# Kernel optimization log

Hardware: AMD Instinct MI355X
Metric: run time of the kernel (lower is better)

Reference implementation:

```python
import jax, jax.numpy as jnp
import numpy as np

D_IN = 1024
D_OUT = 1024
NUM_HEADS = 16
HEAD_DIM = D_OUT // NUM_HEADS


def setup_inputs() -> dict:
    key = jax.random.key(0)
    k_x, k_q, k_k, k_v, k_o, k_ob = jax.random.split(key, 6)
    s_in = 1.0 / np.sqrt(D_IN)
    s_out = 1.0 / np.sqrt(D_OUT)
    return {
        "x": jax.random.normal(k_x, (2, 2048, D_IN), dtype=jnp.float32),
        "W_q": jax.random.uniform(k_q, (D_IN, D_OUT), minval=-s_in, maxval=s_in, dtype=jnp.float32),
        "W_k": jax.random.uniform(k_k, (D_IN, D_OUT), minval=-s_in, maxval=s_in, dtype=jnp.float32),
        "W_v": jax.random.uniform(k_v, (D_IN, D_OUT), minval=-s_in, maxval=s_in, dtype=jnp.float32),
        "W_out": jax.random.uniform(k_o, (D_OUT, D_OUT), minval=-s_out, maxval=s_out, dtype=jnp.float32),
        "b_out": jax.random.uniform(k_ob, (D_OUT,), minval=-s_out, maxval=s_out, dtype=jnp.float32),
    }


def reference(x, W_q, W_k, W_v, W_out, b_out):
    b, t, _ = x.shape
    # projections (qkv_bias=False)
    q = (x @ W_q).reshape(b, t, NUM_HEADS, HEAD_DIM).transpose(0, 2, 1, 3)  # [b,h,t,d]
    k = (x @ W_k).reshape(b, t, NUM_HEADS, HEAD_DIM).transpose(0, 2, 1, 3)
    v = (x @ W_v).reshape(b, t, NUM_HEADS, HEAD_DIM).transpose(0, 2, 1, 3)
    scale = 1.0 / np.sqrt(HEAD_DIM).astype(np.float32)
    scores = jnp.einsum("bhqd,bhkd->bhqk", q, k) * scale  # [b,h,t,t]
    causal = jnp.triu(jnp.ones((t, t), dtype=bool), k=1)
    scores = jnp.where(causal, -jnp.inf, scores)
    weights = jax.nn.softmax(scores, axis=-1)
    # dropout p=0.0 -> identity
    context = jnp.einsum("bhqk,bhkd->bhqd", weights, v)
    context = context.transpose(0, 2, 1, 3).reshape(b, t, D_OUT)
    return context @ W_out + b_out
```

## Files before the change

kernel.cpp:

```cpp
#include <hip/hip_runtime.h>
#include <hip/hip_bf16.h>

#define B_  2
#define T_  2048
#define D_  1024
#define H_  16
#define DH_ 64
#define M_  (B_*T_)

typedef _Float16 f16;
typedef __attribute__((ext_vector_type(4))) _Float16 f16x4;
typedef __attribute__((ext_vector_type(8))) _Float16 f16x8;
typedef __attribute__((ext_vector_type(4))) float f32x4;

#define GLOAD_LDS(gp, lp) __builtin_amdgcn_global_load_lds( \
    (const __attribute__((address_space(1))) void*)(gp),    \
    (__attribute__((address_space(3))) void*)(lp), 16, 0, 0)

__global__ void cvt_x(const float* __restrict__ x, f16* __restrict__ xb) {
  size_t i = ((size_t)blockIdx.x * blockDim.x + threadIdx.x) * 8;
  float4 a = *(const float4*)(x + i);
  float4 b = *(const float4*)(x + i + 4);
  f16x8 o;
  o[0]=(f16)a.x; o[1]=(f16)a.y; o[2]=(f16)a.z; o[3]=(f16)a.w;
  o[4]=(f16)b.x; o[5]=(f16)b.y; o[6]=(f16)b.z; o[7]=(f16)b.w;
  *(f16x8*)(xb + i) = o;
}

__global__ void twt(const float* __restrict__ wq, const float* __restrict__ wk,
                    const float* __restrict__ wv, const float* __restrict__ wo,
                    f16* __restrict__ wqkvT, f16* __restrict__ woutT) {
  int j = blockIdx.z;
  const float* src = (j==0)?wq:(j==1)?wk:(j==2)?wv:wo;
  f16* dst = (j<3) ? (wqkvT + (size_t)j*D_*D_) : woutT;
  __shared__ float tile[32][33];
  int n0 = blockIdx.x*32, k0 = blockIdx.y*32;
  int tx = threadIdx.x, ty = threadIdx.y;
  #pragma unroll
  for (int i=0;i<32;i+=8)
    tile[ty+i][tx] = src[(size_t)(k0+ty+i)*D_ + n0+tx];
  __syncthreads();
  #pragma unroll
  for (int i=0;i<32;i+=8)
    dst[(size_t)(n0+ty+i)*D_ + k0+tx] = (f16)tile[tx][ty+i];
}

__launch_bounds__(256, 2)
__global__ void qkv_gemm(const f16* __restrict__ xb, const f16* __restrict__ wT,
                         f16* __restrict__ Qp, f16* __restrict__ Kp, f16* __restrict__ Vtp) {
  const int j  = blockIdx.z;
  const f16* B0 = wT + (size_t)j * D_ * D_;
  const int m0 = blockIdx.y * 128;
  const int n0 = blockIdx.x * 128;
  __shared__ alignas(16) char smem[128*136*2];
  f16* AsF = (f16*)smem;
  f16* BsF = AsF + 128*64;
  const int tid = threadIdx.x;
  const int lane = tid & 63, wave = tid >> 6;
  const int ln = lane & 15, quad = lane >> 4;
  const int wm = wave >> 1, wn = wave & 1;

  f32x4 acc[4][4];
  #pragma unroll
  for (int a=0;a<4;++a)
    #pragma unroll
    for (int b=0;b<4;++b) acc[a][b] = f32x4{0.f,0.f,0.f,0.f};

  for (int k0 = 0; k0 < D_; k0 += 64) {
    #pragma unroll
    for (int p = 0; p < 4; ++p) {
      int slot = p*256 + tid;
      int row  = slot >> 3;
      int c    = (slot & 7) ^ (row & 7);
      GLOAD_LDS(xb + (size_t)(m0+row)*D_ + k0 + c*8, AsF + (size_t)slot*8);
      GLOAD_LDS(B0 + (size_t)(n0+row)*D_ + k0 + c*8, BsF + (size_t)slot*8);
    }
    __syncthreads();
    #pragma unroll
    for (int ks = 0; ks < 2; ++ks) {
      const int cb = ((ks*4 + quad) ^ (ln & 7)) * 8;
      f16x8 af[4], bf[4];
      #pragma unroll
      for (int mt = 0; mt < 4; ++mt)
        af[mt] = *(const f16x8*)(AsF + (size_t)(wm*64 + mt*16 + ln)*64 + cb);
      #pragma unroll
      for (int nt = 0; nt < 4; ++nt)
        bf[nt] = *(const f16x8*)(BsF + (size_t)(wn*64 + nt*16 + ln)*64 + cb);
      #pragma unroll
      for (int mt = 0; mt < 4; ++mt)
        #pragma unroll
        for (int nt = 0; nt < 4; ++nt)
          acc[mt][nt] = __builtin_amdgcn_mfma_f32_16x16x32_f16(af[mt], bf[nt], acc[mt][nt], 0, 0, 0);
    }
    __syncthreads();
  }

  if (j < 2) {
    #pragma unroll
    for (int mt = 0; mt < 4; ++mt)
      #pragma unroll
      for (int nt = 0; nt < 4; ++nt)
        #pragma unroll
        for (int r = 0; r < 4; ++r) {
          int gm = m0 + wm*64 + mt*16 + quad*4 + r;
          int gn = n0 + wn*64 + nt*16 + ln;
          int bb = gm >> 11, t = gm & (T_-1);
          int h  = gn >> 6,  dd = gn & (DH_-1);
          float v = acc[mt][nt][r];
          size_t idx = ((((size_t)bb*H_ + h)*T_ + t)*DH_) + dd;
          if (j == 0) Qp[idx] = (f16)(v * 0.125f);
          else        Kp[idx] = (f16)v;
        }
  } else {
    __syncthreads();
    f16* VtS = (f16*)smem;
    #pragma unroll
    for (int mt = 0; mt < 4; ++mt)
      #pragma unroll
      for (int nt = 0; nt < 4; ++nt) {
        f16x4 v;
        v[0]=(f16)acc[mt][nt][0]; v[1]=(f16)acc[mt][nt][1];
        v[2]=(f16)acc[mt][nt][2]; v[3]=(f16)acc[mt][nt][3];
        *(f16x4*)&VtS[(size_t)(wn*64 + nt*16 + ln)*136 + wm*64 + mt*16 + quad*4] = v;
      }
    __syncthreads();
    int dd_loc = tid >> 1, half = tid & 1;
    int gn = n0 + dd_loc, h = gn >> 6, dd = gn & (DH_-1);
    int bb = m0 >> 11, tb = (m0 & (T_-1)) + half*64;
    f16* dst = Vtp + ((size_t)(bb*H_ + h)*DH_ + dd)*T_ + tb;
    const f16* src = VtS + (size_t)dd_loc*136 + half*64;
    #pragma unroll
    for (int u = 0; u < 8; ++u)
      *(uint4*)(dst + u*8) = *(const uint4*)(src + u*8);
  }
}

__launch_bounds__(256, 4)
__global__ void flash(const f16* __restrict__ Qp, const f16* __restrict__ Kp,
                      const f16* __restrict__ Vtp, f16* __restrict__ ctx) {
  const int xi = blockIdx.x;
  const int qt = (xi & 1) ? ((xi - 1) >> 1) : (31 - (xi >> 1));
  const int bh = blockIdx.y;
  const int b = bh >> 4, h = bh & (H_-1);
  const size_t headQK = (size_t)bh * T_ * DH_;
  const size_t headV  = (size_t)bh * DH_ * T_;
  const int tid = threadIdx.x, lane = tid & 63, w = tid >> 6;
  const int ln = lane & 15, quad = lane >> 4;
  __shared__ alignas(16) f16 Ks[64][72];
  __shared__ alignas(16) f16 Vs[64][72];
  __shared__ alignas(16) f16 Ps[64][72];

  const int qw = qt*64 + w*16;

  f16x8 qf[2];
  #pragma unroll
  for (int ks = 0; ks < 2; ++ks)
    qf[ks] = *(const f16x8*)&Qp[headQK + (size_t)(qw + ln)*DH_ + ks*32 + quad*8];

  f32x4 o[4];
  #pragma unroll
  for (int dt = 0; dt < 4; ++dt) o[dt] = f32x4{0.f,0.f,0.f,0.f};
  float l_part = 0.f;

  const int srow = tid >> 2, scol = (tid & 3) * 16;
  for (int it = 0; it <= qt; ++it) {
    const int kv0 = it * 64;
    *(uint4*)&Ks[srow][scol]   = *(const uint4*)&Kp[headQK + (size_t)(kv0+srow)*DH_ + scol];
    *(uint4*)&Ks[srow][scol+8] = *(const uint4*)&Kp[headQK + (size_t)(kv0+srow)*DH_ + scol + 8];
    *(uint4*)&Vs[srow][scol]   = *(const uint4*)&Vtp[headV + (size_t)srow*T_ + kv0 + scol];
    *(uint4*)&Vs[srow][scol+8] = *(const uint4*)&Vtp[headV + (size_t)srow*T_ + kv0 + scol + 8];
    __syncthreads();

    f32x4 s[4];
    #pragma unroll
    for (int kt = 0; kt < 4; ++kt) s[kt] = f32x4{0.f,0.f,0.f,0.f};
    #pragma unroll
    for (int ks = 0; ks < 2; ++ks) {
      f16x8 kx[4];
      #pragma unroll
      for (int kt = 0; kt < 4; ++kt)
        kx[kt] = *(const f16x8*)&Ks[kt*16 + ln][ks*32 + quad*8];
      #pragma unroll
      for (int kt = 0; kt < 4; ++kt)
        s[kt] = __builtin_amdgcn_mfma_f32_16x16x32_f16(kx[kt], qf[ks], s[kt], 0, 0, 0);
    }
    if (it == qt) {
      #pragma unroll
      for (int kt = 0; kt < 4; ++kt)
        #pragma unroll
        for (int r = 0; r < 4; ++r)
          if (kv0 + kt*16 + quad*4 + r > qw + ln) s[kt][r] = -INFINITY;
    }
    #pragma unroll
    for (int kt = 0; kt < 4; ++kt) {
      f16x4 pk;
      #pragma unroll
      for (int r = 0; r < 4; ++r) {
        float p = __expf(s[kt][r]);
        l_part += p;
        pk[r] = (f16)p;
      }
      *(f16x4*)&Ps[w*16 + ln][kt*16 + quad*4] = pk;
    }
    asm volatile("" ::: "memory");

    #pragma unroll
    for (int ks = 0; ks < 2; ++ks) {
      f16x8 px = *(const f16x8*)&Ps[w*16 + ln][ks*32 + quad*8];
      #pragma unroll
      for (int dt = 0; dt < 4; ++dt) {
        f16x8 vy = *(const f16x8*)&Vs[dt*16 + ln][ks*32 + quad*8];
        o[dt] = __builtin_amdgcn_mfma_f32_16x16x32_f16(px, vy, o[dt], 0, 0, 0);
      }
    }
    __syncthreads();
  }

  float l = l_part;
  l += __shfl_xor(l, 16, 64);
  l += __shfl_xor(l, 32, 64);
  float inv = 1.0f / l;

  #pragma unroll
  for (int r = 0; r < 4; ++r) {
    float linv = __shfl(inv, quad*4 + r, 64);
    int t = qt*64 + w*16 + quad*4 + r;
    #pragma unroll
    for (int dt = 0; dt < 4; ++dt)
      ctx[(size_t)(b*T_ + t)*D_ + h*DH_ + dt*16 + ln] = (f16)(o[dt][r] * linv);
  }
}

__launch_bounds__(256, 2)
__global__ void out_gemm(const f16* __restrict__ ctx, const f16* __restrict__ woT,
                         const float* __restrict__ bo, float* __restrict__ out) {
  const int m0 = blockIdx.y * 128;
  const int n0 = blockIdx.x * 128;
  __shared__ alignas(16) f16 smem[2*128*64];
  f16* AsF = smem;
  f16* BsF = AsF + 128*64;
  const int tid = threadIdx.x;
  const int lane = tid & 63, wave = tid >> 6;
  const int ln = lane & 15, quad = lane >> 4;
  const int wm = wave >> 1, wn = wave & 1;

  f32x4 acc[4][4];
  #pragma unroll
  for (int a=0;a<4;++a)
    #pragma unroll
    for (int b=0;b<4;++b) acc[a][b] = f32x4{0.f,0.f,0.f,0.f};

  for (int k0 = 0; k0 < D_; k0 += 64) {
    #pragma unroll
    for (int p = 0; p < 4; ++p) {
      int slot = p*256 + tid;
      int row  = slot >> 3;
      int c    = (slot & 7) ^ (row & 7);
      GLOAD_LDS(ctx + (size_t)(m0+row)*D_ + k0 + c*8, AsF + (size_t)slot*8);
      GLOAD_LDS(woT + (size_t)(n0+row)*D_ + k0 + c*8, BsF + (size_t)slot*8);
    }
    __syncthreads();
    #pragma unroll
    for (int ks = 0; ks < 2; ++ks) {
      const int cb = ((ks*4 + quad) ^ (ln & 7)) * 8;
      f16x8 af[4], bf[4];
      #pragma unroll
      for (int mt = 0; mt < 4; ++mt)
        af[mt] = *(const f16x8*)(AsF + (size_t)(wm*64 + mt*16 + ln)*64 + cb);
      #pragma unroll
      for (int nt = 0; nt < 4; ++nt)
        bf[nt] = *(const f16x8*)(BsF + (size_t)(wn*64 + nt*16 + ln)*64 + cb);
      #pragma unroll
      for (int mt = 0; mt < 4; ++mt)
        #pragma unroll
        for (int nt = 0; nt < 4; ++nt)
          acc[mt][nt] = __builtin_amdgcn_mfma_f32_16x16x32_f16(af[mt], bf[nt], acc[mt][nt], 0, 0, 0);
    }
    __syncthreads();
  }

  float bias[4];
  #pragma unroll
  for (int nt = 0; nt < 4; ++nt) bias[nt] = bo[n0 + wn*64 + nt*16 + ln];
  #pragma unroll
  for (int mt = 0; mt < 4; ++mt)
    #pragma unroll
    for (int nt = 0; nt < 4; ++nt)
      #pragma unroll
      for (int r = 0; r < 4; ++r) {
        int gm = m0 + wm*64 + mt*16 + quad*4 + r;
        int gn = n0 + wn*64 + nt*16 + ln;
        out[(size_t)gm*D_ + gn] = acc[mt][nt][r] + bias[nt];
      }
}

extern "C" void kernel_launch(void* const* d_in, const int* in_sizes, int n_in,
                              void* d_out, int out_size, void* d_ws, size_t ws_size,
                              hipStream_t stream) {
  const float* x  = (const float*)d_in[0];
  const float* wq = (const float*)d_in[1];
  const float* wk = (const float*)d_in[2];
  const float* wv = (const float*)d_in[3];
  const float* wo = (const float*)d_in[4];
  const float* bo = (const float*)d_in[5];
  float* out = (float*)d_out;

  f16* ws    = (f16*)d_ws;
  f16* xb    = ws;
  f16* wqkvT = xb    + (size_t)M_*D_;
  f16* woutT = wqkvT + (size_t)3*D_*D_;
  f16* Qb    = woutT + (size_t)D_*D_;
  f16* Kb    = Qb    + (size_t)M_*D_;
  f16* Vb    = Kb    + (size_t)M_*D_;
  f16* ctx   = Vb    + (size_t)M_*D_;

  cvt_x<<<(M_*D_)/(256*8), 256, 0, stream>>>(x, xb);
  twt<<<dim3(D_/32, D_/32, 4), dim3(32, 8), 0, stream>>>(wq, wk, wv, wo, wqkvT, woutT);
  qkv_gemm<<<dim3(D_/128, M_/128, 3), 256, 0, stream>>>(xb, wqkvT, Qb, Kb, Vb);
  flash<<<dim3(32, 32), 256, 0, stream>>>(Qb, Kb, Vb, ctx);
  out_gemm<<<dim3(D_/128, M_/128), 256, 0, stream>>>(ctx, woutT, bo, out);
}
```

Measured before the change: 197.2 us.

## Double-buffer K/V with async LDS loads, pair causal tiles, vectorize GEMM epilogues

The flash kernel now uses double-buffered, XOR-swizzled K/V tiles filled by direct global-to-LDS loads, so the next tile's fetch overlaps the current tile's compute. Each block processes a short and a long causal query tile in turn, halving the grid and balancing work per block. The Q/K projection and output GEMMs swap their MFMA operand order so each lane holds four consecutive columns, allowing vectorized f16x4/float4 stores and a float4 bias load. The costs are more LDS per block and lower occupancy (launch bounds go from 4 to 3), plus fewer total blocks in flight.

```diff
diff --git a/kernel.cpp b/kernel.cpp
--- a/kernel.cpp
+++ b/kernel.cpp
@@ -66,6 +66,7 @@
     #pragma unroll
     for (int b=0;b<4;++b) acc[a][b] = f32x4{0.f,0.f,0.f,0.f};
 
+  const bool swapped = (j < 2);
   for (int k0 = 0; k0 < D_; k0 += 64) {
     #pragma unroll
     for (int p = 0; p < 4; ++p) {
@@ -86,31 +87,39 @@
       #pragma unroll
       for (int nt = 0; nt < 4; ++nt)
         bf[nt] = *(const f16x8*)(BsF + (size_t)(wn*64 + nt*16 + ln)*64 + cb);
-      #pragma unroll
-      for (int mt = 0; mt < 4; ++mt)
+      if (swapped) {
         #pragma unroll
         for (int nt = 0; nt < 4; ++nt)
-          acc[mt][nt] = __builtin_amdgcn_mfma_f32_16x16x32_f16(af[mt], bf[nt], acc[mt][nt], 0, 0, 0);
-    }
-    __syncthreads();
-  }
-
-  if (j < 2) {
-    #pragma unroll
-    for (int mt = 0; mt < 4; ++mt)
-      #pragma unroll
-      for (int nt = 0; nt < 4; ++nt)
-        #pragma unroll
-        for (int r = 0; r < 4; ++r) {
-          int gm = m0 + wm*64 + mt*16 + quad*4 + r;
-          int gn = n0 + wn*64 + nt*16 + ln;
-          int bb = gm >> 11, t = gm & (T_-1);
-          int h  = gn >> 6,  dd = gn & (DH_-1);
-          float v = acc[mt][nt][r];
-          size_t idx = ((((size_t)bb*H_ + h)*T_ + t)*DH_) + dd;
-          if (j == 0) Qp[idx] = (f16)(v * 0.125f);
-          else        Kp[idx] = (f16)v;
-        }
+          #pragma unroll
+          for (int mt = 0; mt < 4; ++mt)
+            acc[nt][mt] = __builtin_amdgcn_mfma_f32_16x16x32_f16(bf[nt], af[mt], acc[nt][mt], 0, 0, 0);
+      } else {
+        #pragma unroll
+        for (int mt = 0; mt < 4; ++mt)
+          #pragma unroll
+          for (int nt = 0; nt < 4; ++nt)
+            acc[mt][nt] = __builtin_amdgcn_mfma_f32_16x16x32_f16(af[mt], bf[nt], acc[mt][nt], 0, 0, 0);
+      }
+    }
+    __syncthreads();
+  }
+
+  if (swapped) {
+    const float scale = (j == 0) ? 0.125f : 1.0f;
+    f16* dstB = (j == 0) ? Qp : Kp;
+    #pragma unroll
+    for (int nt = 0; nt < 4; ++nt)
+      #pragma unroll
+      for (int mt = 0; mt < 4; ++mt) {
+        int gm = m0 + wm*64 + mt*16 + ln;
+        int gn = n0 + wn*64 + nt*16 + quad*4;
+        int bb = gm >> 11, t = gm & (T_-1);
+        int h  = gn >> 6,  dd = gn & (DH_-1);
+        f16x4 v;
+        #pragma unroll
+        for (int r = 0; r < 4; ++r) v[r] = (f16)(acc[nt][mt][r] * scale);
+        *(f16x4*)&dstB[((((size_t)bb*H_ + h)*T_ + t)*DH_) + dd] = v;
+      }
   } else {
     __syncthreads();
     f16* VtS = (f16*)smem;
@@ -135,99 +144,121 @@
   }
 }
 
-__launch_bounds__(256, 4)
+__launch_bounds__(256, 3)
 __global__ void flash(const f16* __restrict__ Qp, const f16* __restrict__ Kp,
                       const f16* __restrict__ Vtp, f16* __restrict__ ctx) {
-  const int xi = blockIdx.x;
-  const int qt = (xi & 1) ? ((xi - 1) >> 1) : (31 - (xi >> 1));
+  const int p  = blockIdx.x;
   const int bh = blockIdx.y;
   const int b = bh >> 4, h = bh & (H_-1);
-  const size_t headQK = (size_t)bh * T_ * DH_;
-  const size_t headV  = (size_t)bh * DH_ * T_;
+  const f16* Kh = Kp  + (size_t)bh * T_ * DH_;
+  const f16* Vh = Vtp + (size_t)bh * DH_ * T_;
+  const f16* Qh = Qp  + (size_t)bh * T_ * DH_;
   const int tid = threadIdx.x, lane = tid & 63, w = tid >> 6;
   const int ln = lane & 15, quad = lane >> 4;
-  __shared__ alignas(16) f16 Ks[64][72];
-  __shared__ alignas(16) f16 Vs[64][72];
+  __shared__ alignas(16) f16 Ks[2*64*64];
+  __shared__ alignas(16) f16 Vs[2*64*64];
   __shared__ alignas(16) f16 Ps[64][72];
 
-  const int qw = qt*64 + w*16;
-
-  f16x8 qf[2];
-  #pragma unroll
-  for (int ks = 0; ks < 2; ++ks)
-    qf[ks] = *(const f16x8*)&Qp[headQK + (size_t)(qw + ln)*DH_ + ks*32 + quad*8];
-
-  f32x4 o[4];
-  #pragma unroll
-  for (int dt = 0; dt < 4; ++dt) o[dt] = f32x4{0.f,0.f,0.f,0.f};
-  float l_part = 0.f;
-
-  const int srow = tid >> 2, scol = (tid & 3) * 16;
-  for (int it = 0; it <= qt; ++it) {
-    const int kv0 = it * 64;
-    *(uint4*)&Ks[srow][scol]   = *(const uint4*)&Kp[headQK + (size_t)(kv0+srow)*DH_ + scol];
-    *(uint4*)&Ks[srow][scol+8] = *(const uint4*)&Kp[headQK + (size_t)(kv0+srow)*DH_ + scol + 8];
-    *(uint4*)&Vs[srow][scol]   = *(const uint4*)&Vtp[headV + (size_t)srow*T_ + kv0 + scol];
-    *(uint4*)&Vs[srow][scol+8] = *(const uint4*)&Vtp[headV + (size_t)srow*T_ + kv0 + scol + 8];
-    __syncthreads();
-
-    f32x4 s[4];
-    #pragma unroll
-    for (int kt = 0; kt < 4; ++kt) s[kt] = f32x4{0.f,0.f,0.f,0.f};
-    #pragma unroll
-    for (int ks = 0; ks < 2; ++ks) {
-      f16x8 kx[4];
-      #pragma unroll
-      for (int kt = 0; kt < 4; ++kt)
-        kx[kt] = *(const f16x8*)&Ks[kt*16 + ln][ks*32 + quad*8];
-      #pragma unroll
-      for (int kt = 0; kt < 4; ++kt)
-        s[kt] = __builtin_amdgcn_mfma_f32_16x16x32_f16(kx[kt], qf[ks], s[kt], 0, 0, 0);
-    }
-    if (it == qt) {
-      #pragma unroll
-      for (int kt = 0; kt < 4; ++kt)
-        #pragma unroll
-        for (int r = 0; r < 4; ++r)
-          if (kv0 + kt*16 + quad*4 + r > qw + ln) s[kt][r] = -INFINITY;
-    }
-    #pragma unroll
-    for (int kt = 0; kt < 4; ++kt) {
-      f16x4 pk;
-      #pragma unroll
-      for (int r = 0; r < 4; ++r) {
-        float p = __expf(s[kt][r]);
-        l_part += p;
-        pk[r] = (f16)p;
-      }
-      *(f16x4*)&Ps[w*16 + ln][kt*16 + quad*4] = pk;
-    }
-    asm volatile("" ::: "memory");
-
-    #pragma unroll
-    for (int ks = 0; ks < 2; ++ks) {
-      f16x8 px = *(const f16x8*)&Ps[w*16 + ln][ks*32 + quad*8];
-      #pragma unroll
-      for (int dt = 0; dt < 4; ++dt) {
-        f16x8 vy = *(const f16x8*)&Vs[dt*16 + ln][ks*32 + quad*8];
-        o[dt] = __builtin_amdgcn_mfma_f32_16x16x32_f16(px, vy, o[dt], 0, 0, 0);
-      }
-    }
-    __syncthreads();
-  }
-
-  float l = l_part;
-  l += __shfl_xor(l, 16, 64);
-  l += __shfl_xor(l, 32, 64);
-  float inv = 1.0f / l;
-
-  #pragma unroll
-  for (int r = 0; r < 4; ++r) {
-    float linv = __shfl(inv, quad*4 + r, 64);
-    int t = qt*64 + w*16 + quad*4 + r;
-    #pragma unroll
-    for (int dt = 0; dt < 4; ++dt)
-      ctx[(size_t)(b*T_ + t)*D_ + h*DH_ + dt*16 + ln] = (f16)(o[dt][r] * linv);
+  #pragma unroll 1
+  for (int phase = 0; phase < 2; ++phase) {
+    const int qt = phase ? (31 - p) : p;
+    const int qw = qt*64 + w*16;
+
+    f16x8 qf[2];
+    #pragma unroll
+    for (int ks = 0; ks < 2; ++ks)
+      qf[ks] = *(const f16x8*)&Qh[(size_t)(qw + ln)*DH_ + ks*32 + quad*8];
+
+    f32x4 o[4];
+    #pragma unroll
+    for (int dt = 0; dt < 4; ++dt) o[dt] = f32x4{0.f,0.f,0.f,0.f};
+    float l_part = 0.f;
+
+    {
+      #pragma unroll
+      for (int i = 0; i < 2; ++i) {
+        int row = w*16 + i*8 + (lane >> 3);
+        int c   = (lane & 7) ^ (row & 7);
+        GLOAD_LDS(Kh + (size_t)row*DH_ + c*8, Ks + (w*128 + i*64 + lane)*8);
+        GLOAD_LDS(Vh + (size_t)row*T_  + c*8, Vs + (w*128 + i*64 + lane)*8);
+      }
+    }
+    __syncthreads();
+
+    for (int it = 0; it <= qt; ++it) {
+      const f16* Kc = Ks + (it & 1)*4096;
+      const f16* Vc = Vs + (it & 1)*4096;
+      if (it < qt) {
+        const int kv1 = (it + 1)*64;
+        f16* Kn = Ks + ((it + 1) & 1)*4096;
+        f16* Vn = Vs + ((it + 1) & 1)*4096;
+        #pragma unroll
+        for (int i = 0; i < 2; ++i) {
+          int row = w*16 + i*8 + (lane >> 3);
+          int c   = (lane & 7) ^ (row & 7);
+          GLOAD_LDS(Kh + (size_t)(kv1 + row)*DH_ + c*8, Kn + (w*128 + i*64 + lane)*8);
+          GLOAD_LDS(Vh + (size_t)row*T_ + kv1 + c*8,    Vn + (w*128 + i*64 + lane)*8);
+        }
+      }
+
+      f32x4 s[4];
+      #pragma unroll
+      for (int kt = 0; kt < 4; ++kt) s[kt] = f32x4{0.f,0.f,0.f,0.f};
+      #pragma unroll
+      for (int ks = 0; ks < 2; ++ks) {
+        f16x8 kx[4];
+        #pragma unroll
+        for (int kt = 0; kt < 4; ++kt)
+          kx[kt] = *(const f16x8*)(Kc + (size_t)(kt*16 + ln)*64 + (((ks*4 + quad) ^ (ln & 7))*8));
+        #pragma unroll
+        for (int kt = 0; kt < 4; ++kt)
+          s[kt] = __builtin_amdgcn_mfma_f32_16x16x32_f16(kx[kt], qf[ks], s[kt], 0, 0, 0);
+      }
+      if (it == qt) {
+        const int kv0 = it*64;
+        #pragma unroll
+        for (int kt = 0; kt < 4; ++kt)
+          #pragma unroll
+          for (int r = 0; r < 4; ++r)
+            if (kv0 + kt*16 + quad*4 + r > qw + ln) s[kt][r] = -INFINITY;
+      }
+      #pragma unroll
+      for (int kt = 0; kt < 4; ++kt) {
+        f16x4 pk;
+        #pragma unroll
+        for (int r = 0; r < 4; ++r) {
+          float pe = __expf(s[kt][r]);
+          l_part += pe;
+          pk[r] = (f16)pe;
+        }
+        *(f16x4*)&Ps[w*16 + ln][kt*16 + quad*4] = pk;
+      }
+      asm volatile("" ::: "memory");
+
+      #pragma unroll
+      for (int ks = 0; ks < 2; ++ks) {
+        f16x8 px = *(const f16x8*)&Ps[w*16 + ln][ks*32 + quad*8];
+        #pragma unroll
+        for (int dt = 0; dt < 4; ++dt) {
+          f16x8 vy = *(const f16x8*)(Vc + (size_t)(dt*16 + ln)*64 + (((ks*4 + quad) ^ (ln & 7))*8));
+          o[dt] = __builtin_amdgcn_mfma_f32_16x16x32_f16(px, vy, o[dt], 0, 0, 0);
+        }
+      }
+      __syncthreads();
+    }
+
+    float l = l_part;
+    l += __shfl_xor(l, 16, 64);
+    l += __shfl_xor(l, 32, 64);
+    float inv = 1.0f / l;
+    #pragma unroll
+    for (int r = 0; r < 4; ++r) {
+      float linv = __shfl(inv, quad*4 + r, 64);
+      int t = qt*64 + w*16 + quad*4 + r;
+      #pragma unroll
+      for (int dt = 0; dt < 4; ++dt)
+        ctx[(size_t)(b*T_ + t)*D_ + h*DH_ + dt*16 + ln] = (f16)(o[dt][r] * linv);
+    }
   }
 }
 
@@ -271,27 +302,29 @@
       for (int nt = 0; nt < 4; ++nt)
         bf[nt] = *(const f16x8*)(BsF + (size_t)(wn*64 + nt*16 + ln)*64 + cb);
       #pragma unroll
-      for (int mt = 0; mt < 4; ++mt)
-        #pragma unroll
-        for (int nt = 0; nt < 4; ++nt)
-          acc[mt][nt] = __builtin_amdgcn_mfma_f32_16x16x32_f16(af[mt], bf[nt], acc[mt][nt], 0, 0, 0);
-    }
-    __syncthreads();
-  }
-
-  float bias[4];
-  #pragma unroll
-  for (int nt = 0; nt < 4; ++nt) bias[nt] = bo[n0 + wn*64 + nt*16 + ln];
-  #pragma unroll
-  for (int mt = 0; mt < 4; ++mt)
-    #pragma unroll
-    for (int nt = 0; nt < 4; ++nt)
-      #pragma unroll
-      for (int r = 0; r < 4; ++r) {
-        int gm = m0 + wm*64 + mt*16 + quad*4 + r;
-        int gn = n0 + wn*64 + nt*16 + ln;
-        out[(size_t)gm*D_ + gn] = acc[mt][nt][r] + bias[nt];
-      }
+      for (int nt = 0; nt < 4; ++nt)
+        #pragma unroll
+        for (int mt = 0; mt < 4; ++mt)
+          acc[nt][mt] = __builtin_amdgcn_mfma_f32_16x16x32_f16(bf[nt], af[mt], acc[nt][mt], 0, 0, 0);
+    }
+    __syncthreads();
+  }
+
+  #pragma unroll
+  for (int nt = 0; nt < 4; ++nt) {
+    int gn = n0 + wn*64 + nt*16 + quad*4;
+    float4 bv = *(const float4*)&bo[gn];
+    #pragma unroll
+    for (int mt = 0; mt < 4; ++mt) {
+      int gm = m0 + wm*64 + mt*16 + ln;
+      float4 v;
+      v.x = acc[nt][mt][0] + bv.x;
+      v.y = acc[nt][mt][1] + bv.y;
+      v.z = acc[nt][mt][2] + bv.z;
+      v.w = acc[nt][mt][3] + bv.w;
+      *(float4*)&out[(size_t)gm*D_ + gn] = v;
+    }
+  }
 }
 
 extern "C" void kernel_launch(void* const* d_in, const int* in_sizes, int n_in,
@@ -317,6 +350,6 @@
   cvt_x<<<(M_*D_)/(256*8), 256, 0, stream>>>(x, xb);
   twt<<<dim3(D_/32, D_/32, 4), dim3(32, 8), 0, stream>>>(wq, wk, wv, wo, wqkvT, woutT);
   qkv_gemm<<<dim3(D_/128, M_/128, 3), 256, 0, stream>>>(xb, wqkvT, Qb, Kb, Vb);
-  flash<<<dim3(32, 32), 256, 0, stream>>>(Qb, Kb, Vb, ctx);
+  flash<<<dim3(16, 32), 256, 0, stream>>>(Qb, Kb, Vb, ctx);
   out_gemm<<<dim3(D_/128, M_/128), 256, 0, stream>>>(ctx, woutT, bo, out);
 }
```

Result: faster. 190.8 us (-3.3%).
